# Kernel tuning notes

Measured on AMD Instinct MI355X. Metric: run time of the kernel, lower is better.

## Reference

```python
import jax, jax.numpy as jnp
import numpy as np

KH, KW = 3, 3
DIL = 2          # path index 1 dilation
G = 4            # deformable groups

def setup_inputs() -> dict:
    key = jax.random.key(0)
    k1, k2, k3, k4 = jax.random.split(key, 4)
    x = jax.random.normal(k1, (2, 256, 132, 132), jnp.float32)
    # offset-predicting conv (72 = deformable_groups * 2 * 3 * 3); small init so offsets are realistic
    offset_w = jax.random.normal(k2, (72, 256, 3, 3), jnp.float32) * 0.01
    offset_b = jax.random.normal(k3, (72,), jnp.float32) * 0.01
    deform_w = jax.random.normal(k4, (256, 256, 3, 3), jnp.float32) * 0.05
    return {"x": x, "offset_w": offset_w, "offset_b": offset_b, "deform_w": deform_w}

def _deform_conv(x, offset, weight):
    # x: [N,C,H,W]; offset: [N, G*2*KH*KW, Ho, Wo]; weight: [Cout, C, KH, KW]
    N, C, H, W = x.shape
    Cout = weight.shape[0]
    Ho = H - DIL * (KH - 1)
    Wo = W - DIL * (KW - 1)
    Cg = C // G
    K = KH * KW
    # mmcv layout: per group, per kernel tap: (dy, dx)
    off = offset.reshape(N, G, K, 2, Ho, Wo)
    dy, dx = off[:, :, :, 0], off[:, :, :, 1]            # [N,G,K,Ho,Wo]
    kk = jnp.arange(K)
    ky, kx = kk // KW, kk % KW
    base_y = ky[:, None] * DIL + jnp.arange(Ho)[None, :]  # [K,Ho]
    base_x = kx[:, None] * DIL + jnp.arange(Wo)[None, :]  # [K,Wo]
    y = dy + base_y[None, None, :, :, None].astype(dy.dtype)
    xx = dx + base_x[None, None, :, None, :].astype(dx.dtype)
    y0f = jnp.floor(y)
    x0f = jnp.floor(xx)
    ly = y - y0f
    lx = xx - x0f
    y0 = y0f.astype(jnp.int32)
    x0 = x0f.astype(jnp.int32)
    img = x.reshape(N, G, Cg, H * W)

    def gather(yi, xi, w):
        valid = (yi >= 0) & (yi < H) & (xi >= 0) & (xi < W)
        idx = jnp.clip(yi, 0, H - 1) * W + jnp.clip(xi, 0, W - 1)   # [N,G,K,Ho,Wo]
        v = jnp.take_along_axis(img, idx.reshape(N, G, 1, -1), axis=3)
        v = v.reshape(N, G, Cg, K, Ho, Wo)
        return v * (w * valid)[:, :, None]

    sampled = (gather(y0,     x0,     (1 - ly) * (1 - lx)) +
               gather(y0,     x0 + 1, (1 - ly) * lx) +
               gather(y0 + 1, x0,     ly * (1 - lx)) +
               gather(y0 + 1, x0 + 1, ly * lx))        # [N,G,Cg,K,Ho,Wo]
    w = weight.reshape(Cout, G, Cg, K)
    return jnp.einsum('ngckhw,ogck->nohw', sampled, w)

def reference(x, offset_w, offset_b, deform_w):
    # eval branch: path 1 (stride 1, dilation 2, pad 0)
    offset = jax.lax.conv_general_dilated(
        x, offset_w, window_strides=(1, 1), padding='VALID',
        rhs_dilation=(DIL, DIL),
        dimension_numbers=('NCHW', 'OIHW', 'NCHW')) + offset_b[None, :, None, None]
    return _deform_conv(x, offset, deform_w)
```

## Files before the change

### kernel.cpp

```cpp
#include <hip/hip_runtime.h>
#include <cstddef>

#define KH   3
#define KW   3
#define DIL  2
#define GRP  4
#define CIN  256
#define COUT 256
#define OCH  72
#define OCP  80
#define HIN  132
#define WIN  132
#define HO   128
#define WO   128
#define CG   64
#define KKT  9
#define WROW 2304
#define HW_IN (HIN*WIN)

typedef __attribute__((ext_vector_type(8))) short short8;
typedef __attribute__((ext_vector_type(4))) float float4v;
typedef __attribute__((ext_vector_type(4))) unsigned short ushort4v;

__device__ __forceinline__ unsigned short f2bf(float f) {
    unsigned int u = __float_as_uint(f);
    u += 0x7FFFu + ((u >> 16) & 1u);
    return (unsigned short)(u >> 16);
}
__device__ __forceinline__ float bf2f(unsigned short h) {
    return __uint_as_float(((unsigned int)h) << 16);
}

__global__ __launch_bounds__(512)
void transpose_kernel(const float* __restrict__ x, float* __restrict__ xt) {
    const int bid = blockIdx.x;
    const int wh_ = bid & 1;
    const int h   = (bid >> 1) % HIN;
    const int n   = bid / (HIN * 2);
    const int w0  = wh_ * 66;

    const float* xn = x + (size_t)n * CIN * HW_IN + (size_t)h * WIN;
    float* xo = xt + ((size_t)n * HW_IN + (size_t)h * WIN) * CIN;

#pragma unroll 1
    for (int i = 0; i < 33; ++i) {
        int s = i * 512 + threadIdx.x;
        int c = s & 255;
        int w = w0 + (s >> 8);
        xo[(size_t)w * CIN + c] = xn[(size_t)c * HW_IN + w];
    }
}

__global__ __launch_bounds__(512)
void wprep_kernel(const float* __restrict__ dw,
                  unsigned short* __restrict__ wh,
                  unsigned short* __restrict__ wl) {
    int tid = blockIdx.x * 512 + threadIdx.x;
    if (tid >= COUT * WROW) return;
    int oc  = tid / WROW;
    int rem = tid - oc * WROW;
    int cin = rem / KKT;
    int tap = rem - cin * KKT;
    int g   = cin >> 6;
    int c   = cin & 63;
    float v = dw[tid];
    unsigned short hi = f2bf(v);
    unsigned short lo = f2bf(v - bf2f(hi));
    size_t o = (((size_t)oc * GRP + g) * KKT + tap) * 64 + c;
    wh[o] = hi;
    wl[o] = lo;
}

__global__ __launch_bounds__(512)
void owprep_kernel(const float* __restrict__ ow,
                   unsigned short* __restrict__ owh,
                   unsigned short* __restrict__ owl) {
    int tid = blockIdx.x * 512 + threadIdx.x;
    if (tid >= OCP * WROW) return;
    int oc  = tid / WROW;
    int rem = tid - oc * WROW;
    int q   = rem >> 6;
    int c   = rem & 63;
    int cb  = q / 9;
    int tap = q - cb * 9;
    float v = (oc < OCH) ? ow[((size_t)oc * CIN + cb * 64 + c) * KKT + tap] : 0.f;
    unsigned short hi = f2bf(v);
    owh[tid] = hi;
    owl[tid] = f2bf(v - bf2f(hi));
}

__global__ __launch_bounds__(256, 2)
void offset_mfma_kernel(const float* __restrict__ xt,
                        const unsigned short* __restrict__ owh,
                        const unsigned short* __restrict__ owl,
                        const float* __restrict__ b,
                        float* __restrict__ off) {
    const int l   = ((blockIdx.x & 7) << 6) | (blockIdx.x >> 3);
    const int h   = l & 1;
    const int y   = (l >> 1) & 127;
    const int n   = l >> 8;
    const int px0 = h * 64;

    const int t    = threadIdx.x;
    const int lane = t & 63;
    const int w4   = __builtin_amdgcn_readfirstlane(t >> 6);
    const int l15  = lane & 15;
    const int kgrp8 = (lane >> 4) << 3;

    __shared__ unsigned short Ah[2][4096], Al[2][4096];
    __shared__ unsigned short Bh[2][5120], Bl[2][5120];

    float4v acc[5];
#pragma unroll
    for (int nt = 0; nt < 5; ++nt) acc[nt] = (float4v)0.f;

    const float* xtn = xt + (size_t)n * HW_IN * CIN;

    auto stageA = [&](int bb, int q) {
        const int cb = q / 9, tap = q - cb * 9;
        const int ky = tap / 3, kx = tap - ky * 3;
        const int cq = t & 15;
#pragma unroll
        for (int i = 0; i < 4; ++i) {
            int pp = i * 16 + (t >> 4);
            const float* src = xtn + ((size_t)(y + 2 * ky) * WIN + (px0 + pp + 2 * kx)) * CIN
                             + cb * 64 + cq * 4;
            float4v v = *(const float4v*)src;
            ushort4v hv, lv;
#pragma unroll
            for (int j = 0; j < 4; ++j) {
                unsigned short hi = f2bf(v[j]);
                hv[j] = hi;
                lv[j] = f2bf(v[j] - bf2f(hi));
            }
            int idx = pp * 64 + ((cq * 4) ^ ((pp & 7) << 3));
            *(ushort4v*)&Ah[bb][idx] = hv;
            *(ushort4v*)&Al[bb][idx] = lv;
        }
    };

    auto stageB = [&](int bb, int q) {
#pragma unroll
        for (int i = 0; i < 3; ++i) {
            int s = t + i * 256;
            if (s < 640) {
                int oc = s >> 3, c8 = (s & 7) * 8;
                size_t wo = (size_t)oc * WROW + q * 64 + c8;
                short8 hv = *(const short8*)(owh + wo);
                short8 lv = *(const short8*)(owl + wo);
                int idx = oc * 64 + (c8 ^ ((oc & 7) << 3));
                *(short8*)&Bh[bb][idx] = hv;
                *(short8*)&Bl[bb][idx] = lv;
            }
        }
    };

    stageA(0, 0);
    stageB(0, 0);
    __syncthreads();

#pragma unroll 1
    for (int q = 0; q < 36; ++q) {
        const int buf = q & 1;
        if (q + 1 < 36) { stageA(buf ^ 1, q + 1); stageB(buf ^ 1, q + 1); }

#pragma unroll
        for (int ks = 0; ks < 2; ++ks) {
            const int kl = ks * 32 + kgrp8;
            const int ppa = w4 * 16 + l15;
            const int ai  = ppa * 64 + (kl ^ ((ppa & 7) << 3));
            short8 Ahf = *(const short8*)&Ah[buf][ai];
            short8 Alf = *(const short8*)&Al[buf][ai];
#pragma unroll
            for (int nt = 0; nt < 5; ++nt) {
                const int oc = nt * 16 + l15;
                const int bi = oc * 64 + (kl ^ ((oc & 7) << 3));
                short8 Bhf = *(const short8*)&Bh[buf][bi];
                short8 Blf = *(const short8*)&Bl[buf][bi];
                acc[nt] = __builtin_amdgcn_mfma_f32_16x16x32_bf16(Ahf, Bhf, acc[nt], 0, 0, 0);
                acc[nt] = __builtin_amdgcn_mfma_f32_16x16x32_bf16(Ahf, Blf, acc[nt], 0, 0, 0);
                acc[nt] = __builtin_amdgcn_mfma_f32_16x16x32_bf16(Alf, Bhf, acc[nt], 0, 0, 0);
            }
        }
        __syncthreads();
    }

    const int pxr = (lane >> 4) * 4;
#pragma unroll
    for (int nt = 0; nt < 5; ++nt) {
        const int oc = nt * 16 + l15;
        if (oc < OCH) {
            float bias = b[oc];
            float4v v = acc[nt];
#pragma unroll
            for (int j = 0; j < 4; ++j) v[j] += bias;
            *(float4v*)&off[((size_t)(n * OCH + oc) * HO + y) * WO + px0 + w4 * 16 + pxr] = v;
        }
    }
}

__global__ __launch_bounds__(512, 4)
void deform_kernel(const float* __restrict__ xt,
                   const float* __restrict__ off,
                   const unsigned short* __restrict__ wh,
                   const unsigned short* __restrict__ wl,
                   float* __restrict__ out) {
    const int l   = ((blockIdx.x & 7) << 6) | (blockIdx.x >> 3);
    const int h   = l & 1;
    const int y   = (l >> 1) & 127;
    const int n   = l >> 8;
    const int px0 = h * 64;

    const int t    = threadIdx.x;
    const int lane = t & 63;
    const int w8   = t >> 6;
    const int oc_base = __builtin_amdgcn_readfirstlane(w8) * 32;
    const int l15  = lane & 15;
    const int kgrp8 = (lane >> 4) << 3;

    __shared__ float cw[4][KKT][65];
    __shared__ int   ci[4][KKT][65];
    __shared__ unsigned short Ah[2][4096];
    __shared__ unsigned short Al[2][4096];

    float4v acc[4][2];
#pragma unroll
    for (int mt = 0; mt < 4; ++mt)
#pragma unroll
        for (int nt = 0; nt < 2; ++nt)
            acc[mt][nt] = (float4v)0.f;

    const float* xtn = xt + (size_t)n * HW_IN * CIN;
    const int s_cq = t & 15;

    size_t wrow[2];
#pragma unroll
    for (int nt = 0; nt < 2; ++nt)
        wrow[nt] = (size_t)(oc_base + nt * 16 + l15) * WROW;

    short8 Bch[2][2], Bcl[2][2], Bnh[2][2], Bnl[2][2];

    auto loadB = [&](int g, int tap, short8 (&Bh_)[2][2], short8 (&Bl_)[2][2]) {
        const int gt = (g * KKT + tap) * 64;
#pragma unroll
        for (int ks = 0; ks < 2; ++ks)
#pragma unroll
            for (int nt = 0; nt < 2; ++nt) {
                size_t wo = wrow[nt] + gt + ks * 32 + kgrp8;
                Bh_[ks][nt] = *(const short8*)(wh + wo);
                Bl_[ks][nt] = *(const short8*)(wl + wo);
            }
    };

    auto stage = [&](int bb, int g, int tap) {
        const float* xg = xtn + g * 64 + s_cq * 4;
#pragma unroll
        for (int i = 0; i < 2; ++i) {
            int pp = i * 32 + (t >> 4);
            float4v s0 = *(const float4v*)(xg + (size_t)ci[0][tap][pp] * CIN);
            float4v s1 = *(const float4v*)(xg + (size_t)ci[1][tap][pp] * CIN);
            float4v s2 = *(const float4v*)(xg + (size_t)ci[2][tap][pp] * CIN);
            float4v s3 = *(const float4v*)(xg + (size_t)ci[3][tap][pp] * CIN);
            float w0 = cw[0][tap][pp], w1 = cw[1][tap][pp];
            float w2 = cw[2][tap][pp], w3 = cw[3][tap][pp];
            ushort4v hv, lv;
#pragma unroll
            for (int j = 0; j < 4; ++j) {
                float v = w0 * s0[j] + w1 * s1[j] + w2 * s2[j] + w3 * s3[j];
                unsigned short hi = f2bf(v);
                hv[j] = hi;
                lv[j] = f2bf(v - bf2f(hi));
            }
            int idx = pp * 64 + ((s_cq * 4) ^ ((pp & 7) << 3));
            *(ushort4v*)&Ah[bb][idx] = hv;
            *(ushort4v*)&Al[bb][idx] = lv;
        }
    };

#pragma unroll 1
    for (int g = 0; g < GRP; ++g) {
#pragma unroll
        for (int i = 0; i < 2; ++i) {
            int s = t + i * 512;
            if (s < KKT * 64) {
                int tap = s >> 6;
                int pp  = s & 63;
                int ky = tap / 3, kx = tap - ky * 3;
                size_t obase = ((size_t)(n * OCH + g * 18 + tap * 2) * HO + y) * WO + px0 + pp;
                float dy = off[obase];
                float dx = off[obase + (size_t)HO * WO];
                float fy = dy + (float)(ky * DIL + y);
                float fx = dx + (float)(kx * DIL + px0 + pp);
                float y0f = floorf(fy), x0f = floorf(fx);
                float ly = fy - y0f,   lx = fx - x0f;
                int iy0 = (int)y0f, ix0 = (int)x0f;
                int iy1 = iy0 + 1,  ix1 = ix0 + 1;
                float vy0 = (iy0 >= 0 && iy0 < HIN) ? 1.f : 0.f;
                float vy1 = (iy1 >= 0 && iy1 < HIN) ? 1.f : 0.f;
                float vx0 = (ix0 >= 0 && ix0 < WIN) ? 1.f : 0.f;
                float vx1 = (ix1 >= 0 && ix1 < WIN) ? 1.f : 0.f;
                int iy0c = min(max(iy0, 0), HIN - 1);
                int iy1c = min(max(iy1, 0), HIN - 1);
                int ix0c = min(max(ix0, 0), WIN - 1);
                int ix1c = min(max(ix1, 0), WIN - 1);
                cw[0][tap][pp] = (1.f - ly) * (1.f - lx) * vy0 * vx0;
                cw[1][tap][pp] = (1.f - ly) * lx * vy0 * vx1;
                cw[2][tap][pp] = ly * (1.f - lx) * vy1 * vx0;
                cw[3][tap][pp] = ly * lx * vy1 * vx1;
                ci[0][tap][pp] = iy0c * WIN + ix0c;
                ci[1][tap][pp] = iy0c * WIN + ix1c;
                ci[2][tap][pp] = iy1c * WIN + ix0c;
                ci[3][tap][pp] = iy1c * WIN + ix1c;
            }
        }
        __syncthreads();

        stage(0, g, 0);
        loadB(g, 0, Bch, Bcl);
        __syncthreads();

        for (int tap = 0; tap < KKT; ++tap) {
            const int buf = tap & 1;
            if (tap + 1 < KKT) {
                stage(buf ^ 1, g, tap + 1);
                loadB(g, tap + 1, Bnh, Bnl);
            }

#pragma unroll
            for (int ks = 0; ks < 2; ++ks) {
                const int kl = ks * 32 + kgrp8;
                short8 Ahf[4], Alf[4];
#pragma unroll
                for (int mt = 0; mt < 4; ++mt) {
                    int pp = mt * 16 + l15;
                    int ai = pp * 64 + (kl ^ ((pp & 7) << 3));
                    Ahf[mt] = *(const short8*)&Ah[buf][ai];
                    Alf[mt] = *(const short8*)&Al[buf][ai];
                }
#pragma unroll
                for (int mt = 0; mt < 4; ++mt)
#pragma unroll
                    for (int nt = 0; nt < 2; ++nt) {
                        acc[mt][nt] = __builtin_amdgcn_mfma_f32_16x16x32_bf16(
                            Ahf[mt], Bch[ks][nt], acc[mt][nt], 0, 0, 0);
                        acc[mt][nt] = __builtin_amdgcn_mfma_f32_16x16x32_bf16(
                            Ahf[mt], Bcl[ks][nt], acc[mt][nt], 0, 0, 0);
                        acc[mt][nt] = __builtin_amdgcn_mfma_f32_16x16x32_bf16(
                            Alf[mt], Bch[ks][nt], acc[mt][nt], 0, 0, 0);
                    }
            }

            if (tap + 1 < KKT) {
#pragma unroll
                for (int ks = 0; ks < 2; ++ks)
#pragma unroll
                    for (int nt = 0; nt < 2; ++nt) {
                        Bch[ks][nt] = Bnh[ks][nt];
                        Bcl[ks][nt] = Bnl[ks][nt];
                    }
            }
            __syncthreads();
        }
    }

    const int pxr = (lane >> 4) * 4;
#pragma unroll
    for (int nt = 0; nt < 2; ++nt) {
        const int oc = oc_base + nt * 16 + l15;
        size_t ob = ((size_t)(n * COUT + oc) * HO + y) * WO + px0;
#pragma unroll
        for (int mt = 0; mt < 4; ++mt)
            *(float4v*)&out[ob + mt * 16 + pxr] = acc[mt][nt];
    }
}

extern "C" void kernel_launch(void* const* d_in, const int* in_sizes, int n_in,
                              void* d_out, int out_size, void* d_ws, size_t ws_size,
                              hipStream_t stream) {
    const float* x  = (const float*)d_in[0];
    const float* ow = (const float*)d_in[1];
    const float* ob = (const float*)d_in[2];
    const float* dw = (const float*)d_in[3];
    float* out = (float*)d_out;

    char* base = (char*)d_ws;
    float* off = (float*)base;
    unsigned short* wh  = (unsigned short*)(base + 9437184);
    unsigned short* wl  = (unsigned short*)(base + 9437184 + 1179648);
    float* xt           = (float*)(base + 9437184 + 2 * 1179648);
    unsigned short* owh = (unsigned short*)(base + 9437184 + 2 * 1179648 + 35721216);
    unsigned short* owl = (unsigned short*)(base + 9437184 + 2 * 1179648 + 35721216 + 368640);

    wprep_kernel<<<1152, 512, 0, stream>>>(dw, wh, wl);
    owprep_kernel<<<360, 512, 0, stream>>>(ow, owh, owl);
    transpose_kernel<<<528, 512, 0, stream>>>(x, xt);
    offset_mfma_kernel<<<512, 256, 0, stream>>>(xt, owh, owl, ob, off);
    deform_kernel<<<512, 512, 0, stream>>>(xt, off, wh, wl, out);
}
```

Baseline: 408.2 us.

## Drop low-half weight split, retile offset conv, and use LDS-tiled transpose

Weights for both the offset and deformable convolutions are now stored as a single bf16 value with no low residual, so each MMA step runs two instead of three bf16 MFMAs and half the weight traffic is removed. The activations still get a hi/lo split. The offset conv is retiled to 32-pixel blocks with the output-channel padding raised to 96, and B fragments are loaded straight from global memory into registers instead of through shared memory. The NCHW to NHWC transpose now goes through a padded LDS tile so both reads and writes are coalesced. Dropping the weight residual lowers precision, which could matter most for the offset prediction because the bilinear sampling positions depend on it.

```diff
diff --git a/kernel.cpp b/kernel.cpp
--- a/kernel.cpp
+++ b/kernel.cpp
@@ -8,7 +8,7 @@
 #define CIN  256
 #define COUT 256
 #define OCH  72
-#define OCP  80
+#define OCP  96
 #define HIN  132
 #define WIN  132
 #define HO   128
@@ -31,30 +31,43 @@
     return __uint_as_float(((unsigned int)h) << 16);
 }
 
-__global__ __launch_bounds__(512)
+__global__ __launch_bounds__(256)
 void transpose_kernel(const float* __restrict__ x, float* __restrict__ xt) {
     const int bid = blockIdx.x;
-    const int wh_ = bid & 1;
-    const int h   = (bid >> 1) % HIN;
-    const int n   = bid / (HIN * 2);
-    const int w0  = wh_ * 66;
+    const int wt  = bid % 5;
+    const int h   = (bid / 5) % HIN;
+    const int n   = bid / (5 * HIN);
+    const int w0  = wt * 32;
+    const int t   = threadIdx.x;
+
+    __shared__ float ld[32][257];
 
     const float* xn = x + (size_t)n * CIN * HW_IN + (size_t)h * WIN;
+    {
+        const int w  = t & 31;
+        const int c0 = t >> 5;
+        if (w0 + w < WIN) {
+#pragma unroll
+            for (int i = 0; i < 32; ++i) {
+                int c = i * 8 + c0;
+                ld[w][c] = xn[(size_t)c * HW_IN + w0 + w];
+            }
+        }
+    }
+    __syncthreads();
+
     float* xo = xt + ((size_t)n * HW_IN + (size_t)h * WIN) * CIN;
-
-#pragma unroll 1
-    for (int i = 0; i < 33; ++i) {
-        int s = i * 512 + threadIdx.x;
-        int c = s & 255;
-        int w = w0 + (s >> 8);
-        xo[(size_t)w * CIN + c] = xn[(size_t)c * HW_IN + w];
+    const int c = t;
+#pragma unroll
+    for (int w = 0; w < 32; ++w) {
+        if (w0 + w < WIN)
+            xo[(size_t)(w0 + w) * CIN + c] = ld[w][c];
     }
 }
 
 __global__ __launch_bounds__(512)
 void wprep_kernel(const float* __restrict__ dw,
-                  unsigned short* __restrict__ wh,
-                  unsigned short* __restrict__ wl) {
+                  unsigned short* __restrict__ wh) {
     int tid = blockIdx.x * 512 + threadIdx.x;
     if (tid >= COUT * WROW) return;
     int oc  = tid / WROW;
@@ -63,18 +76,13 @@
     int tap = rem - cin * KKT;
     int g   = cin >> 6;
     int c   = cin & 63;
-    float v = dw[tid];
-    unsigned short hi = f2bf(v);
-    unsigned short lo = f2bf(v - bf2f(hi));
     size_t o = (((size_t)oc * GRP + g) * KKT + tap) * 64 + c;
-    wh[o] = hi;
-    wl[o] = lo;
+    wh[o] = f2bf(dw[tid]);
 }
 
 __global__ __launch_bounds__(512)
 void owprep_kernel(const float* __restrict__ ow,
-                   unsigned short* __restrict__ owh,
-                   unsigned short* __restrict__ owl) {
+                   unsigned short* __restrict__ owh) {
     int tid = blockIdx.x * 512 + threadIdx.x;
     if (tid >= OCP * WROW) return;
     int oc  = tid / WROW;
@@ -84,45 +92,43 @@
     int cb  = q / 9;
     int tap = q - cb * 9;
     float v = (oc < OCH) ? ow[((size_t)oc * CIN + cb * 64 + c) * KKT + tap] : 0.f;
-    unsigned short hi = f2bf(v);
-    owh[tid] = hi;
-    owl[tid] = f2bf(v - bf2f(hi));
-}
-
-__global__ __launch_bounds__(256, 2)
+    owh[tid] = f2bf(v);
+}
+
+__global__ __launch_bounds__(256, 4)
 void offset_mfma_kernel(const float* __restrict__ xt,
                         const unsigned short* __restrict__ owh,
-                        const unsigned short* __restrict__ owl,
                         const float* __restrict__ b,
                         float* __restrict__ off) {
-    const int l   = ((blockIdx.x & 7) << 6) | (blockIdx.x >> 3);
-    const int h   = l & 1;
-    const int y   = (l >> 1) & 127;
-    const int n   = l >> 8;
-    const int px0 = h * 64;
+    const int l   = ((blockIdx.x & 7) << 7) | (blockIdx.x >> 3);
+    const int q   = l & 3;
+    const int y   = (l >> 2) & 127;
+    const int n   = l >> 9;
+    const int px0 = q * 32;
 
     const int t    = threadIdx.x;
     const int lane = t & 63;
-    const int w4   = __builtin_amdgcn_readfirstlane(t >> 6);
+    const int w4   = t >> 6;
+    const int mt   = w4 & 1;
+    const int nh   = __builtin_amdgcn_readfirstlane(w4 >> 1);
     const int l15  = lane & 15;
     const int kgrp8 = (lane >> 4) << 3;
 
-    __shared__ unsigned short Ah[2][4096], Al[2][4096];
-    __shared__ unsigned short Bh[2][5120], Bl[2][5120];
-
-    float4v acc[5];
-#pragma unroll
-    for (int nt = 0; nt < 5; ++nt) acc[nt] = (float4v)0.f;
+    __shared__ unsigned short Ah[2][2048], Al[2][2048];
+
+    float4v acc[3];
+#pragma unroll
+    for (int nt = 0; nt < 3; ++nt) acc[nt] = (float4v)0.f;
 
     const float* xtn = xt + (size_t)n * HW_IN * CIN;
 
-    auto stageA = [&](int bb, int q) {
-        const int cb = q / 9, tap = q - cb * 9;
+    auto stageA = [&](int bb, int qc) {
+        const int cb = qc / 9, tap = qc - cb * 9;
         const int ky = tap / 3, kx = tap - ky * 3;
         const int cq = t & 15;
 #pragma unroll
-        for (int i = 0; i < 4; ++i) {
-            int pp = i * 16 + (t >> 4);
+        for (int i = 0; i < 2; ++i) {
+            int pp = (t >> 4) + 16 * i;
             const float* src = xtn + ((size_t)(y + 2 * ky) * WIN + (px0 + pp + 2 * kx)) * CIN
                              + cb * 64 + cq * 4;
             float4v v = *(const float4v*)src;
@@ -139,62 +145,58 @@
         }
     };
 
-    auto stageB = [&](int bb, int q) {
-#pragma unroll
-        for (int i = 0; i < 3; ++i) {
-            int s = t + i * 256;
-            if (s < 640) {
-                int oc = s >> 3, c8 = (s & 7) * 8;
-                size_t wo = (size_t)oc * WROW + q * 64 + c8;
-                short8 hv = *(const short8*)(owh + wo);
-                short8 lv = *(const short8*)(owl + wo);
-                int idx = oc * 64 + (c8 ^ ((oc & 7) << 3));
-                *(short8*)&Bh[bb][idx] = hv;
-                *(short8*)&Bl[bb][idx] = lv;
-            }
-        }
+    short8 Bc[2][3], Bn[2][3];
+    auto loadB = [&](int qc, short8 (&B)[2][3]) {
+#pragma unroll
+        for (int ks = 0; ks < 2; ++ks)
+#pragma unroll
+            for (int nt = 0; nt < 3; ++nt) {
+                int oc = nh * 48 + nt * 16 + l15;
+                B[ks][nt] = *(const short8*)(owh + (size_t)oc * WROW + qc * 64 + ks * 32 + kgrp8);
+            }
     };
 
     stageA(0, 0);
-    stageB(0, 0);
+    loadB(0, Bc);
     __syncthreads();
 
 #pragma unroll 1
-    for (int q = 0; q < 36; ++q) {
-        const int buf = q & 1;
-        if (q + 1 < 36) { stageA(buf ^ 1, q + 1); stageB(buf ^ 1, q + 1); }
+    for (int qc = 0; qc < 36; ++qc) {
+        const int buf = qc & 1;
+        if (qc + 1 < 36) { stageA(buf ^ 1, qc + 1); loadB(qc + 1, Bn); }
 
 #pragma unroll
         for (int ks = 0; ks < 2; ++ks) {
-            const int kl = ks * 32 + kgrp8;
-            const int ppa = w4 * 16 + l15;
+            const int kl  = ks * 32 + kgrp8;
+            const int ppa = mt * 16 + l15;
             const int ai  = ppa * 64 + (kl ^ ((ppa & 7) << 3));
             short8 Ahf = *(const short8*)&Ah[buf][ai];
             short8 Alf = *(const short8*)&Al[buf][ai];
 #pragma unroll
-            for (int nt = 0; nt < 5; ++nt) {
-                const int oc = nt * 16 + l15;
-                const int bi = oc * 64 + (kl ^ ((oc & 7) << 3));
-                short8 Bhf = *(const short8*)&Bh[buf][bi];
-                short8 Blf = *(const short8*)&Bl[buf][bi];
-                acc[nt] = __builtin_amdgcn_mfma_f32_16x16x32_bf16(Ahf, Bhf, acc[nt], 0, 0, 0);
-                acc[nt] = __builtin_amdgcn_mfma_f32_16x16x32_bf16(Ahf, Blf, acc[nt], 0, 0, 0);
-                acc[nt] = __builtin_amdgcn_mfma_f32_16x16x32_bf16(Alf, Bhf, acc[nt], 0, 0, 0);
-            }
+            for (int nt = 0; nt < 3; ++nt) {
+                acc[nt] = __builtin_amdgcn_mfma_f32_16x16x32_bf16(Ahf, Bc[ks][nt], acc[nt], 0, 0, 0);
+                acc[nt] = __builtin_amdgcn_mfma_f32_16x16x32_bf16(Alf, Bc[ks][nt], acc[nt], 0, 0, 0);
+            }
+        }
+        if (qc + 1 < 36) {
+#pragma unroll
+            for (int ks = 0; ks < 2; ++ks)
+#pragma unroll
+                for (int nt = 0; nt < 3; ++nt) Bc[ks][nt] = Bn[ks][nt];
         }
         __syncthreads();
     }
 
     const int pxr = (lane >> 4) * 4;
 #pragma unroll
-    for (int nt = 0; nt < 5; ++nt) {
-        const int oc = nt * 16 + l15;
+    for (int nt = 0; nt < 3; ++nt) {
+        const int oc = nh * 48 + nt * 16 + l15;
         if (oc < OCH) {
             float bias = b[oc];
             float4v v = acc[nt];
 #pragma unroll
             for (int j = 0; j < 4; ++j) v[j] += bias;
-            *(float4v*)&off[((size_t)(n * OCH + oc) * HO + y) * WO + px0 + w4 * 16 + pxr] = v;
+            *(float4v*)&off[((size_t)(n * OCH + oc) * HO + y) * WO + px0 + mt * 16 + pxr] = v;
         }
     }
 }
@@ -203,7 +205,6 @@
 void deform_kernel(const float* __restrict__ xt,
                    const float* __restrict__ off,
                    const unsigned short* __restrict__ wh,
-                   const unsigned short* __restrict__ wl,
                    float* __restrict__ out) {
     const int l   = ((blockIdx.x & 7) << 6) | (blockIdx.x >> 3);
     const int h   = l & 1;
@@ -238,18 +239,15 @@
     for (int nt = 0; nt < 2; ++nt)
         wrow[nt] = (size_t)(oc_base + nt * 16 + l15) * WROW;
 
-    short8 Bch[2][2], Bcl[2][2], Bnh[2][2], Bnl[2][2];
-
-    auto loadB = [&](int g, int tap, short8 (&Bh_)[2][2], short8 (&Bl_)[2][2]) {
+    short8 Bch[2][2], Bnh[2][2];
+
+    auto loadB = [&](int g, int tap, short8 (&B)[2][2]) {
         const int gt = (g * KKT + tap) * 64;
 #pragma unroll
         for (int ks = 0; ks < 2; ++ks)
 #pragma unroll
-            for (int nt = 0; nt < 2; ++nt) {
-                size_t wo = wrow[nt] + gt + ks * 32 + kgrp8;
-                Bh_[ks][nt] = *(const short8*)(wh + wo);
-                Bl_[ks][nt] = *(const short8*)(wl + wo);
-            }
+            for (int nt = 0; nt < 2; ++nt)
+                B[ks][nt] = *(const short8*)(wh + wrow[nt] + gt + ks * 32 + kgrp8);
     };
 
     auto stage = [&](int bb, int g, int tap) {
@@ -316,14 +314,14 @@
         __syncthreads();
 
         stage(0, g, 0);
-        loadB(g, 0, Bch, Bcl);
+        loadB(g, 0, Bch);
         __syncthreads();
 
         for (int tap = 0; tap < KKT; ++tap) {
             const int buf = tap & 1;
             if (tap + 1 < KKT) {
                 stage(buf ^ 1, g, tap + 1);
-                loadB(g, tap + 1, Bnh, Bnl);
+                loadB(g, tap + 1, Bnh);
             }
 
 #pragma unroll
@@ -344,8 +342,6 @@
                         acc[mt][nt] = __builtin_amdgcn_mfma_f32_16x16x32_bf16(
                             Ahf[mt], Bch[ks][nt], acc[mt][nt], 0, 0, 0);
                         acc[mt][nt] = __builtin_amdgcn_mfma_f32_16x16x32_bf16(
-                            Ahf[mt], Bcl[ks][nt], acc[mt][nt], 0, 0, 0);
-                        acc[mt][nt] = __builtin_amdgcn_mfma_f32_16x16x32_bf16(
                             Alf[mt], Bch[ks][nt], acc[mt][nt], 0, 0, 0);
                     }
             }
@@ -354,10 +350,8 @@
 #pragma unroll
                 for (int ks = 0; ks < 2; ++ks)
 #pragma unroll
-                    for (int nt = 0; nt < 2; ++nt) {
+                    for (int nt = 0; nt < 2; ++nt)
                         Bch[ks][nt] = Bnh[ks][nt];
-                        Bcl[ks][nt] = Bnl[ks][nt];
-                    }
             }
             __syncthreads();
         }
@@ -384,16 +378,14 @@
     float* out = (float*)d_out;
 
     char* base = (char*)d_ws;
-    float* off = (float*)base;
+    float* off          = (float*)base;
     unsigned short* wh  = (unsigned short*)(base + 9437184);
-    unsigned short* wl  = (unsigned short*)(base + 9437184 + 1179648);
-    float* xt           = (float*)(base + 9437184 + 2 * 1179648);
-    unsigned short* owh = (unsigned short*)(base + 9437184 + 2 * 1179648 + 35721216);
-    unsigned short* owl = (unsigned short*)(base + 9437184 + 2 * 1179648 + 35721216 + 368640);
-
-    wprep_kernel<<<1152, 512, 0, stream>>>(dw, wh, wl);
-    owprep_kernel<<<360, 512, 0, stream>>>(ow, owh, owl);
-    transpose_kernel<<<528, 512, 0, stream>>>(x, xt);
-    offset_mfma_kernel<<<512, 256, 0, stream>>>(xt, owh, owl, ob, off);
-    deform_kernel<<<512, 512, 0, stream>>>(xt, off, wh, wl, out);
-}
+    float* xt           = (float*)(base + 9437184 + 1179648);
+    unsigned short* owh = (unsigned short*)(base + 9437184 + 1179648 + 35721216);
+
+    wprep_kernel<<<1152, 512, 0, stream>>>(dw, wh);
+    owprep_kernel<<<432, 512, 0, stream>>>(ow, owh);
+    transpose_kernel<<<1320, 256, 0, stream>>>(x, xt);
+    offset_mfma_kernel<<<1024, 256, 0, stream>>>(xt, owh, ob, off);
+    deform_kernel<<<512, 512, 0, stream>>>(xt, off, wh, out);
+}
```

After: 333.4 us. -18.3%, faster.
